# Kernel optimization log

Measured on AMD Instinct MI355X. Metric: run time of the kernel, lower is better.

## Reference

```python
import jax, jax.numpy as jnp
import numpy as np

DEFAULT_MASK_VALUE = -0.7 * float(jnp.finfo(jnp.dtype('float32')).max)

B, T, NQ, NKV, D = 2, 1024, 32, 8, 128


def setup_inputs() -> dict:
    key = jax.random.key(0)
    k1, k2, k3, k4 = jax.random.split(key, 4)
    query = jax.random.normal(k1, (B, T, NQ, D), dtype=jnp.float32)
    kk = jax.random.normal(k2, (B, T, NKV, D), dtype=jnp.float32)
    vv = jax.random.normal(k3, (B, T, NKV, D), dtype=jnp.float32)
    # packed-sequence segment ids, sorted so each segment is contiguous (values 1..3, >0 = active)
    decoder_segment_ids = jnp.sort(jax.random.randint(k4, (B, T), 1, 4), axis=-1).astype(jnp.int32)
    return {"query": query, "key": kk, "value": vv,
            "decoder_segment_ids": decoder_segment_ids}


def _attention(query, key, value, decoder_segment_ids):
    # MaxText AttentionOp.apply_attention_dot (prefill / train mode), GQA layout.
    b, t, n, d = query.shape
    n_kv = key.shape[2]
    g = n // n_kv
    q = query.reshape(b, t, n_kv, g, d)
    # qk product: [b, n_kv, g, t, s]
    logits = jnp.einsum('btkgd,bskd->bkgts', q, key)
    # generate_attention_mask: segment mask AND causal mask
    seg_mask = decoder_segment_ids[:, :, None] == decoder_segment_ids[:, None, :]  # [b,t,s]
    row_ids = jax.lax.broadcasted_iota(jnp.int32, (t, t), 0)
    col_ids = jax.lax.broadcasted_iota(jnp.int32, (t, t), 1)
    causal = col_ids <= row_ids  # [t,s]
    mask = jnp.logical_and(seg_mask, causal[None])  # [b,t,s]
    # apply_mask_to_logits: replace masked entries with DEFAULT_MASK_VALUE (avoids add fusion)
    masked = jnp.where(mask[:, None, None, :, :], logits, DEFAULT_MASK_VALUE)
    probs = jax.nn.softmax(masked, axis=-1)
    out = jnp.einsum('bkgts,bskd->btkgd', probs, value)
    return out.reshape(b, t, n, d)


def reference(query, key, value, decoder_segment_ids):
    return _attention(query, key, value, decoder_segment_ids)
```

## Files before the change

kernel.cpp:

```cpp
#include <hip/hip_runtime.h>

constexpr int B_  = 2;
constexpr int T_  = 1024;
constexpr int NQ  = 32;
constexpr int NKV = 8;
constexpr int D_  = 128;

constexpr int BM = 64;
constexpr int BN = 64;
constexpr int NTILE = T_ / BM;
constexpr float MASK_NEG = -3.0e38f;

typedef _Float16 f16;
typedef __fp16 fp16_2 __attribute__((ext_vector_type(2)));
typedef f16 f16x4 __attribute__((ext_vector_type(4)));
typedef f16 f16x8 __attribute__((ext_vector_type(8)));
typedef float floatx4 __attribute__((ext_vector_type(4)));
typedef unsigned int uintx4 __attribute__((ext_vector_type(4)));

__device__ __align__(16) f16 g_K16 [(size_t)B_ * NKV * T_ * D_];
__device__ __align__(16) f16 g_Vt16[(size_t)B_ * NKV * T_ * D_];

__device__ __forceinline__ void dma16(const f16* g, const f16* l) {
    __builtin_amdgcn_global_load_lds(
        (const __attribute__((address_space(1))) void*)g,
        (__attribute__((address_space(3))) void*)l, 16, 0, 0);
}

__device__ __forceinline__ void swap32(unsigned &a, unsigned &b) {
    unsigned ax = (unsigned)__shfl_xor((int)a, 32);
    unsigned bx = (unsigned)__shfl_xor((int)b, 32);
    const bool hi = (threadIdx.x & 32) != 0;
    unsigned na = hi ? bx : a;
    unsigned nb = hi ? b  : ax;
    a = na; b = nb;
}

__device__ __forceinline__ void swap16(unsigned &a, unsigned &b) {
    unsigned ax = (unsigned)__shfl_xor((int)a, 16);
    unsigned bx = (unsigned)__shfl_xor((int)b, 16);
    const bool odd = (threadIdx.x & 16) != 0;
    unsigned na = odd ? bx : a;
    unsigned nb = odd ? b  : ax;
    a = na; b = nb;
}

__device__ __forceinline__ unsigned pk2(float a, float b) {
    union { fp16_2 h; unsigned u; } c;
    c.h = __builtin_amdgcn_cvt_pkrtz(a, b);
    return c.u;
}

__global__ __launch_bounds__(256)
void prep_kernel(const float* __restrict__ K, const float* __restrict__ V) {
    __shared__ f16 lv[64][136];
    const int sblk = blockIdx.x;
    const int kv   = blockIdx.y;
    const int b    = blockIdx.z;
    const int tid  = threadIdx.x;
    const int s0   = sblk * 64;
    const size_t inbase = ((size_t)b * T_) * NKV * D_ + (size_t)kv * D_;

    f16* kout = g_K16 + ((size_t)(b * NKV + kv) * T_ + s0) * D_;
#pragma unroll
    for (int p = 0; p < 4; ++p) {
        const int u = tid + 256 * p;
        const int s = u >> 4, ch = u & 15;
        const float* src = K + inbase + (size_t)(s0 + s) * NKV * D_ + ch * 8;
        float4 f0 = *(const float4*)src;
        float4 f1 = *(const float4*)(src + 4);
        f16x8 hh;
        hh[0] = (f16)f0.x; hh[1] = (f16)f0.y; hh[2] = (f16)f0.z; hh[3] = (f16)f0.w;
        hh[4] = (f16)f1.x; hh[5] = (f16)f1.y; hh[6] = (f16)f1.z; hh[7] = (f16)f1.w;
        *(f16x8*)(kout + s * D_ + ((ch ^ (s & 7)) * 8)) = hh;
    }
#pragma unroll
    for (int p = 0; p < 8; ++p) {
        const int u = tid + 256 * p;
        const int s = u >> 5, d4 = u & 31;
        float4 f = *(const float4*)(V + inbase + (size_t)(s0 + s) * NKV * D_ + d4 * 4);
        f16x4 hh; hh[0] = (f16)f.x; hh[1] = (f16)f.y; hh[2] = (f16)f.z; hh[3] = (f16)f.w;
        *(f16x4*)&lv[s][d4 * 4] = hh;
    }
    __syncthreads();
    f16* vout = g_Vt16 + (size_t)((b * NKV + kv) * 16 + sblk) * 8192;
#pragma unroll
    for (int p = 0; p < 4; ++p) {
        const int u = tid + 256 * p;
        const int d = u >> 3, cu = u & 7;
        f16x8 hh;
#pragma unroll
        for (int j = 0; j < 8; ++j) hh[j] = lv[cu * 8 + j][d];
        *(f16x8*)(vout + d * 64 + ((cu ^ (d & 7)) * 8)) = hh;
    }
}

#define FA_BODY(RK, RV, WK, WV, blkv)                                          \
    {                                                                          \
        const int s0 = (blkv) * BN;                                            \
        __syncthreads();                                                       \
        if ((blkv) + 1 < nblk) {                                               \
            const f16* kt = kbase + (size_t)((blkv) + 1) * 8192 + glane;       \
            const f16* vt = vbase + (size_t)((blkv) + 1) * 8192 + glane;       \
            _Pragma("unroll")                                                  \
            for (int i = 0; i < 4; ++i) {                                      \
                dma16(kt + i * 512, WK + wbase + i * 512);                     \
                dma16(vt + i * 512, WV + wbase + i * 512);                     \
            }                                                                  \
        }                                                                      \
        floatx4 sc[4];                                                         \
        _Pragma("unroll")                                                      \
        for (int nt = 0; nt < 4; ++nt) {                                       \
            floatx4 acc = floatx4{0.f, 0.f, 0.f, 0.f};                         \
            _Pragma("unroll")                                                  \
            for (int c = 0; c < 4; ++c) {                                      \
                f16x8 kf = *(const f16x8*)(RK + (nt * 16 + ln) * 128 + kpc[c]);\
                acc = __builtin_amdgcn_mfma_f32_16x16x32_f16(kf, qfrag[c], acc, 0, 0, 0); \
            }                                                                  \
            sc[nt] = acc;                                                      \
        }                                                                      \
        _Pragma("unroll")                                                      \
        for (int nt = 0; nt < 4; ++nt) {                                       \
            _Pragma("unroll")                                                  \
            for (int r = 0; r < 4; ++r) {                                      \
                const int s = s0 + nt * 16 + quad * 4 + r;                     \
                const bool ok = (s <= qrow_l) && (s >= fs_l);                  \
                sc[nt][r] = ok ? sc[nt][r] : MASK_NEG;                         \
            }                                                                  \
        }                                                                      \
        float mx = fmaxf(                                                      \
            fmaxf(fmaxf(fmaxf(sc[0][0], sc[0][1]), fmaxf(sc[0][2], sc[0][3])), \
                  fmaxf(fmaxf(sc[1][0], sc[1][1]), fmaxf(sc[1][2], sc[1][3]))),\
            fmaxf(fmaxf(fmaxf(sc[2][0], sc[2][1]), fmaxf(sc[2][2], sc[2][3])), \
                  fmaxf(fmaxf(sc[3][0], sc[3][1]), fmaxf(sc[3][2], sc[3][3]))));\
        mx = fmaxf(mx, __shfl_xor(mx, 16));                                    \
        mx = fmaxf(mx, __shfl_xor(mx, 32));                                    \
        const float mnew = fmaxf(m_i, mx);                                     \
        const float av = __expf(m_i - mnew);                                   \
        m_i = mnew;                                                            \
        _Pragma("unroll")                                                      \
        for (int nt = 0; nt < 4; ++nt) {                                       \
            sc[nt][0] = __expf(sc[nt][0] - mnew);                              \
            sc[nt][1] = __expf(sc[nt][1] - mnew);                              \
            sc[nt][2] = __expf(sc[nt][2] - mnew);                              \
            sc[nt][3] = __expf(sc[nt][3] - mnew);                              \
        }                                                                      \
        const int avi = __float_as_int(av);                                    \
        floatx4 avr;                                                           \
        _Pragma("unroll")                                                      \
        for (int r = 0; r < 4; ++r)                                            \
            avr[r] = __int_as_float(__builtin_amdgcn_ds_bpermute(bpbase + 4 * r, avi)); \
        _Pragma("unroll")                                                      \
        for (int dt = 0; dt < 9; ++dt) o_acc[dt] *= avr;                       \
        unsigned Da[4], Db[4];                                                 \
        _Pragma("unroll")                                                      \
        for (int nt = 0; nt < 4; ++nt) {                                       \
            Da[nt] = pk2(sc[nt][0], sc[nt][1]);                                \
            Db[nt] = pk2(sc[nt][2], sc[nt][3]);                                \
        }                                                                      \
        swap32(Da[0], Da[1]); swap32(Db[0], Db[1]);                            \
        swap16(Da[0], Da[1]); swap16(Db[0], Db[1]);                            \
        swap32(Da[2], Da[3]); swap32(Db[2], Db[3]);                            \
        swap16(Da[2], Da[3]); swap16(Db[2], Db[3]);                            \
        union { uintx4 u; f16x8 h; } c0_, c1_;                                 \
        c0_.u = uintx4{Da[0], Db[0], Da[1], Db[1]};                            \
        c1_.u = uintx4{Da[2], Db[2], Da[3], Db[3]};                            \
        const f16x8 af0 = c0_.h;                                               \
        const f16x8 af1 = c1_.h;                                               \
        _Pragma("unroll")                                                      \
        for (int dt = 0; dt < 8; ++dt) {                                       \
            const f16* vr = RV + (dt * 16 + ln) * 64;                          \
            f16x8 b0 = *(const f16x8*)(vr + pc0);                              \
            f16x8 b1 = *(const f16x8*)(vr + pc1);                              \
            o_acc[dt] = __builtin_amdgcn_mfma_f32_16x16x32_f16(af0, b0, o_acc[dt], 0, 0, 0); \
            o_acc[dt] = __builtin_amdgcn_mfma_f32_16x16x32_f16(af1, b1, o_acc[dt], 0, 0, 0); \
        }                                                                      \
        o_acc[8] = __builtin_amdgcn_mfma_f32_16x16x32_f16(af0, vones, o_acc[8], 0, 0, 0); \
        o_acc[8] = __builtin_amdgcn_mfma_f32_16x16x32_f16(af1, vones, o_acc[8], 0, 0, 0); \
    }

__global__ __launch_bounds__(256, 2)
void fa_kernel(const float* __restrict__ Qg, const int* __restrict__ seg,
               float* __restrict__ Og) {
    __shared__ __align__(16) f16 kb0[64 * 128];
    __shared__ __align__(16) f16 kb1[64 * 128];
    __shared__ __align__(16) f16 vb0[128 * 64];
    __shared__ __align__(16) f16 vb1[128 * 64];
    __shared__ int lds_seg[T_];

    const int pair = blockIdx.x;
    const int h    = blockIdx.y;
    const int b    = blockIdx.z;
    const int kv   = h >> 2;

    const int tid  = threadIdx.x;
    const int wave = tid >> 6;
    const int lane = tid & 63;
    const int quad = lane >> 4;
    const int ln   = lane & 15;
    const int sw   = ln & 7;

    int kpc[4];
#pragma unroll
    for (int c = 0; c < 4; ++c) kpc[c] = ((4 * c + quad) ^ sw) * 8;
    const int pc0 = (quad ^ sw) * 8;
    const int pc1 = ((quad + 4) ^ sw) * 8;
    const int bpbase = quad << 4;

    const int glane = wave * 2048 + lane * 8;
    const int wbase = wave * 2048;

    const f16* kbase = g_K16 + (size_t)(b * NKV + kv) * T_ * D_;
    const f16* vbase = g_Vt16 + (size_t)(b * NKV + kv) * T_ * D_;

    *(int4*)&lds_seg[tid * 4] = *(const int4*)(seg + b * T_ + tid * 4);

    f16x8 vones;
#pragma unroll
    for (int j = 0; j < 8; ++j) vones[j] = (f16)1.0f;

    for (int sub = 0; sub < 2; ++sub) {
        const int tile = sub ? pair : (NTILE - 1 - pair);
        const int t0 = tile * BM;

        const int qrow = t0 + wave * 16 + ln;
        const float* qptr = Qg + (((size_t)b * T_ + qrow) * NQ + h) * D_;
        f16x8 qfrag[4];
#pragma unroll
        for (int c = 0; c < 4; ++c) {
            const float* p = qptr + c * 32 + quad * 8;
            float4 f0 = *(const float4*)(p);
            float4 f1 = *(const float4*)(p + 4);
            f16x8 v;
            v[0] = (f16)f0.x; v[1] = (f16)f0.y; v[2] = (f16)f0.z; v[3] = (f16)f0.w;
            v[4] = (f16)f1.x; v[5] = (f16)f1.y; v[6] = (f16)f1.z; v[7] = (f16)f1.w;
            qfrag[c] = v;
        }

        __syncthreads();

        int trow[4];
#pragma unroll
        for (int r = 0; r < 4; ++r) trow[r] = t0 + wave * 16 + quad * 4 + r;

        const int qrow_l = qrow;
        const int segq_l = lds_seg[qrow_l];
        int lo = 0, hi = qrow_l;
        while (lo < hi) {
            const int mid = (lo + hi) >> 1;
            if (lds_seg[mid] < segq_l) lo = mid + 1; else hi = mid;
        }
        const int fs_l = lo;

        const int seg_lo = lds_seg[t0];
        unsigned long long bal = __ballot(lds_seg[lane * 16 + 15] < seg_lo);
        const int blk_start = __popcll(bal) >> 2;
        const int nblk = tile + 1;

        float  m_i = -1.0e30f;
        floatx4 o_acc[9];
#pragma unroll
        for (int dt = 0; dt < 9; ++dt) o_acc[dt] = floatx4{0.f, 0.f, 0.f, 0.f};

        {
            const f16* kt = kbase + (size_t)blk_start * 8192 + glane;
            const f16* vt = vbase + (size_t)blk_start * 8192 + glane;
#pragma unroll
            for (int i = 0; i < 4; ++i) {
                dma16(kt + i * 512, kb0 + wbase + i * 512);
                dma16(vt + i * 512, vb0 + wbase + i * 512);
            }
        }

        int blk = blk_start;
        while (true) {
            FA_BODY(kb0, vb0, kb1, vb1, blk)
            if (++blk >= nblk) break;
            FA_BODY(kb1, vb1, kb0, vb0, blk)
            if (++blk >= nblk) break;
        }

#pragma unroll
        for (int r = 0; r < 4; ++r) {
            const float inv = 1.0f / o_acc[8][r];
            float* optr = Og + (((size_t)b * T_ + trow[r]) * NQ + h) * D_ + ln;
#pragma unroll
            for (int dt = 0; dt < 8; ++dt)
                optr[dt * 16] = o_acc[dt][r] * inv;
        }
    }
}

extern "C" void kernel_launch(void* const* d_in, const int* in_sizes, int n_in,
                              void* d_out, int out_size, void* d_ws, size_t ws_size,
                              hipStream_t stream) {
    const float* Q   = (const float*)d_in[0];
    const float* K   = (const float*)d_in[1];
    const float* V   = (const float*)d_in[2];
    const int*   seg = (const int*)d_in[3];
    float* out = (float*)d_out;

    dim3 pgrid(NTILE, NKV, B_);
    prep_kernel<<<pgrid, 256, 0, stream>>>(K, V);

    dim3 grid(NTILE / 2, NQ, B_);
    fa_kernel<<<grid, 256, 0, stream>>>(Q, seg, out);
}
```

Measured before the change: 124.6 us.

## Load V directly from global into registers, one tile per block, skip masks/rescales

The attention kernel stops staging V through LDS. Each wave now loads V fragments from global memory into registers and computes PV with transposed 16x16x16 MFMAs, so the score-to-operand lane shuffles and the ones-column row-sum MFMA go away, replaced by an explicit shuffle-reduced l_i. The grid now launches one query tile per block with a rotated tile mapping in place of paired tiles, and occupancy is raised to 4 blocks per SM. The mask is skipped for fully valid blocks, and rescaling is skipped when the running max does not change. The trade-off is higher global/L2 traffic for V and more register pressure in exchange for less LDS use and higher occupancy.

```diff
diff --git a/kernel.cpp b/kernel.cpp
--- a/kernel.cpp
+++ b/kernel.cpp
@@ -16,7 +16,6 @@
 typedef f16 f16x4 __attribute__((ext_vector_type(4)));
 typedef f16 f16x8 __attribute__((ext_vector_type(8)));
 typedef float floatx4 __attribute__((ext_vector_type(4)));
-typedef unsigned int uintx4 __attribute__((ext_vector_type(4)));
 
 __device__ __align__(16) f16 g_K16 [(size_t)B_ * NKV * T_ * D_];
 __device__ __align__(16) f16 g_Vt16[(size_t)B_ * NKV * T_ * D_];
@@ -25,24 +24,6 @@
     __builtin_amdgcn_global_load_lds(
         (const __attribute__((address_space(1))) void*)g,
         (__attribute__((address_space(3))) void*)l, 16, 0, 0);
-}
-
-__device__ __forceinline__ void swap32(unsigned &a, unsigned &b) {
-    unsigned ax = (unsigned)__shfl_xor((int)a, 32);
-    unsigned bx = (unsigned)__shfl_xor((int)b, 32);
-    const bool hi = (threadIdx.x & 32) != 0;
-    unsigned na = hi ? bx : a;
-    unsigned nb = hi ? b  : ax;
-    a = na; b = nb;
-}
-
-__device__ __forceinline__ void swap16(unsigned &a, unsigned &b) {
-    unsigned ax = (unsigned)__shfl_xor((int)a, 16);
-    unsigned bx = (unsigned)__shfl_xor((int)b, 16);
-    const bool odd = (threadIdx.x & 16) != 0;
-    unsigned na = odd ? bx : a;
-    unsigned nb = odd ? b  : ax;
-    a = na; b = nb;
 }
 
 __device__ __forceinline__ unsigned pk2(float a, float b) {
@@ -91,22 +72,28 @@
         f16x8 hh;
 #pragma unroll
         for (int j = 0; j < 8; ++j) hh[j] = lv[cu * 8 + j][d];
-        *(f16x8*)(vout + d * 64 + ((cu ^ (d & 7)) * 8)) = hh;
-    }
-}
-
-#define FA_BODY(RK, RV, WK, WV, blkv)                                          \
+        *(f16x8*)(vout + d * 64 + cu * 8) = hh;
+    }
+}
+
+#define FA_BODY(RK, WK, blkv)                                                  \
     {                                                                          \
         const int s0 = (blkv) * BN;                                            \
         __syncthreads();                                                       \
+                 \
+        const f16* vg = vbase + (size_t)(blkv) * 8192 + vofs;                  \
+        f16x4 vf[8][4];                                                        \
+        _Pragma("unroll")                                                      \
+        for (int dt = 0; dt < 8; ++dt) {                                       \
+            _Pragma("unroll")                                                  \
+            for (int nt = 0; nt < 4; ++nt)                                     \
+                vf[dt][nt] = *(const f16x4*)(vg + dt * 1024 + nt * 16);        \
+        }                                                                      \
         if ((blkv) + 1 < nblk) {                                               \
             const f16* kt = kbase + (size_t)((blkv) + 1) * 8192 + glane;       \
-            const f16* vt = vbase + (size_t)((blkv) + 1) * 8192 + glane;       \
-            _Pragma("unroll")                                                  \
-            for (int i = 0; i < 4; ++i) {                                      \
+            _Pragma("unroll")                                                  \
+            for (int i = 0; i < 4; ++i)                                        \
                 dma16(kt + i * 512, WK + wbase + i * 512);                     \
-                dma16(vt + i * 512, WV + wbase + i * 512);                     \
-            }                                                                  \
         }                                                                      \
         floatx4 sc[4];                                                         \
         _Pragma("unroll")                                                      \
@@ -119,13 +106,17 @@
             }                                                                  \
             sc[nt] = acc;                                                      \
         }                                                                      \
-        _Pragma("unroll")                                                      \
-        for (int nt = 0; nt < 4; ++nt) {                                       \
-            _Pragma("unroll")                                                  \
-            for (int r = 0; r < 4; ++r) {                                      \
-                const int s = s0 + nt * 16 + quad * 4 + r;                     \
-                const bool ok = (s <= qrow_l) && (s >= fs_l);                  \
-                sc[nt][r] = ok ? sc[nt][r] : MASK_NEG;                         \
+        \
+        const bool doMask = !__all((s0 >= fs_l) && (s0 + 63 <= qrow_l));       \
+        if (doMask) {                                                          \
+            _Pragma("unroll")                                                  \
+            for (int nt = 0; nt < 4; ++nt) {                                   \
+                _Pragma("unroll")                                              \
+                for (int r = 0; r < 4; ++r) {                                  \
+                    const int s = s0 + nt * 16 + quad * 4 + r;                 \
+                    const bool ok = (s <= qrow_l) && (s >= fs_l);              \
+                    sc[nt][r] = ok ? sc[nt][r] : MASK_NEG;                     \
+                }                                                              \
             }                                                                  \
         }                                                                      \
         float mx = fmaxf(                                                      \
@@ -136,8 +127,14 @@
         mx = fmaxf(mx, __shfl_xor(mx, 16));                                    \
         mx = fmaxf(mx, __shfl_xor(mx, 32));                                    \
         const float mnew = fmaxf(m_i, mx);                                     \
-        const float av = __expf(m_i - mnew);                                   \
-        m_i = mnew;                                                            \
+                   \
+        if (!__all(mx <= m_i)) {                                               \
+            const float av = __expf(m_i - mnew);                               \
+            m_i = mnew;                                                        \
+            l_i *= av;                                                         \
+            _Pragma("unroll")                                                  \
+            for (int dt = 0; dt < 8; ++dt) o_acc[dt] *= av;                    \
+        }                                                                      \
         _Pragma("unroll")                                                      \
         for (int nt = 0; nt < 4; ++nt) {                                       \
             sc[nt][0] = __expf(sc[nt][0] - mnew);                              \
@@ -145,53 +142,44 @@
             sc[nt][2] = __expf(sc[nt][2] - mnew);                              \
             sc[nt][3] = __expf(sc[nt][3] - mnew);                              \
         }                                                                      \
-        const int avi = __float_as_int(av);                                    \
-        floatx4 avr;                                                           \
-        _Pragma("unroll")                                                      \
-        for (int r = 0; r < 4; ++r)                                            \
-            avr[r] = __int_as_float(__builtin_amdgcn_ds_bpermute(bpbase + 4 * r, avi)); \
-        _Pragma("unroll")                                                      \
-        for (int dt = 0; dt < 9; ++dt) o_acc[dt] *= avr;                       \
-        unsigned Da[4], Db[4];                                                 \
+                                         \
+        floatx4 t01 = sc[0] + sc[1], t23 = sc[2] + sc[3];                      \
+        floatx4 tq  = t01 + t23;                                               \
+        float ts = (tq[0] + tq[1]) + (tq[2] + tq[3]);                          \
+        ts += __shfl_xor(ts, 16);                                              \
+        ts += __shfl_xor(ts, 32);                                              \
+        l_i += ts;                                                             \
+        f16x4 pf[4];                                                           \
         _Pragma("unroll")                                                      \
         for (int nt = 0; nt < 4; ++nt) {                                       \
-            Da[nt] = pk2(sc[nt][0], sc[nt][1]);                                \
-            Db[nt] = pk2(sc[nt][2], sc[nt][3]);                                \
-        }                                                                      \
-        swap32(Da[0], Da[1]); swap32(Db[0], Db[1]);                            \
-        swap16(Da[0], Da[1]); swap16(Db[0], Db[1]);                            \
-        swap32(Da[2], Da[3]); swap32(Db[2], Db[3]);                            \
-        swap16(Da[2], Da[3]); swap16(Db[2], Db[3]);                            \
-        union { uintx4 u; f16x8 h; } c0_, c1_;                                 \
-        c0_.u = uintx4{Da[0], Db[0], Da[1], Db[1]};                            \
-        c1_.u = uintx4{Da[2], Db[2], Da[3], Db[3]};                            \
-        const f16x8 af0 = c0_.h;                                               \
-        const f16x8 af1 = c1_.h;                                               \
+            union { unsigned u[2]; f16x4 h; } pu;                              \
+            pu.u[0] = pk2(sc[nt][0], sc[nt][1]);                               \
+            pu.u[1] = pk2(sc[nt][2], sc[nt][3]);                               \
+            pf[nt] = pu.h;                                                     \
+        }                                                                      \
+        __builtin_amdgcn_s_setprio(1);                                         \
         _Pragma("unroll")                                                      \
         for (int dt = 0; dt < 8; ++dt) {                                       \
-            const f16* vr = RV + (dt * 16 + ln) * 64;                          \
-            f16x8 b0 = *(const f16x8*)(vr + pc0);                              \
-            f16x8 b1 = *(const f16x8*)(vr + pc1);                              \
-            o_acc[dt] = __builtin_amdgcn_mfma_f32_16x16x32_f16(af0, b0, o_acc[dt], 0, 0, 0); \
-            o_acc[dt] = __builtin_amdgcn_mfma_f32_16x16x32_f16(af1, b1, o_acc[dt], 0, 0, 0); \
-        }                                                                      \
-        o_acc[8] = __builtin_amdgcn_mfma_f32_16x16x32_f16(af0, vones, o_acc[8], 0, 0, 0); \
-        o_acc[8] = __builtin_amdgcn_mfma_f32_16x16x32_f16(af1, vones, o_acc[8], 0, 0, 0); \
-    }
-
-__global__ __launch_bounds__(256, 2)
+            _Pragma("unroll")                                                  \
+            for (int nt = 0; nt < 4; ++nt)                                     \
+                o_acc[dt] = __builtin_amdgcn_mfma_f32_16x16x16f16(vf[dt][nt], pf[nt], o_acc[dt], 0, 0, 0); \
+        }                                                                      \
+        __builtin_amdgcn_s_setprio(0);                                         \
+    }
+
+__global__ __launch_bounds__(256, 4)
 void fa_kernel(const float* __restrict__ Qg, const int* __restrict__ seg,
                float* __restrict__ Og) {
     __shared__ __align__(16) f16 kb0[64 * 128];
     __shared__ __align__(16) f16 kb1[64 * 128];
-    __shared__ __align__(16) f16 vb0[128 * 64];
-    __shared__ __align__(16) f16 vb1[128 * 64];
     __shared__ int lds_seg[T_];
 
-    const int pair = blockIdx.x;
-    const int h    = blockIdx.y;
-    const int b    = blockIdx.z;
-    const int kv   = h >> 2;
+    const int x = blockIdx.x, y = blockIdx.y, b = blockIdx.z;
+    int u = (x + (y & 15)) & 15;
+    if (b) u = (u + 8) & 15;
+    const int tile = (y & 16) ? (15 - u) : u;
+    const int h  = y;
+    const int kv = h >> 2;
 
     const int tid  = threadIdx.x;
     const int wave = tid >> 6;
@@ -203,9 +191,7 @@
     int kpc[4];
 #pragma unroll
     for (int c = 0; c < 4; ++c) kpc[c] = ((4 * c + quad) ^ sw) * 8;
-    const int pc0 = (quad ^ sw) * 8;
-    const int pc1 = ((quad + 4) ^ sw) * 8;
-    const int bpbase = quad << 4;
+    const int vofs = ln * 64 + quad * 4;
 
     const int glane = wave * 2048 + lane * 8;
     const int wbase = wave * 2048;
@@ -215,78 +201,66 @@
 
     *(int4*)&lds_seg[tid * 4] = *(const int4*)(seg + b * T_ + tid * 4);
 
-    f16x8 vones;
-#pragma unroll
-    for (int j = 0; j < 8; ++j) vones[j] = (f16)1.0f;
-
-    for (int sub = 0; sub < 2; ++sub) {
-        const int tile = sub ? pair : (NTILE - 1 - pair);
-        const int t0 = tile * BM;
-
-        const int qrow = t0 + wave * 16 + ln;
-        const float* qptr = Qg + (((size_t)b * T_ + qrow) * NQ + h) * D_;
-        f16x8 qfrag[4];
-#pragma unroll
-        for (int c = 0; c < 4; ++c) {
-            const float* p = qptr + c * 32 + quad * 8;
-            float4 f0 = *(const float4*)(p);
-            float4 f1 = *(const float4*)(p + 4);
-            f16x8 v;
-            v[0] = (f16)f0.x; v[1] = (f16)f0.y; v[2] = (f16)f0.z; v[3] = (f16)f0.w;
-            v[4] = (f16)f1.x; v[5] = (f16)f1.y; v[6] = (f16)f1.z; v[7] = (f16)f1.w;
-            qfrag[c] = v;
-        }
-
-        __syncthreads();
-
-        int trow[4];
-#pragma unroll
-        for (int r = 0; r < 4; ++r) trow[r] = t0 + wave * 16 + quad * 4 + r;
-
-        const int qrow_l = qrow;
-        const int segq_l = lds_seg[qrow_l];
-        int lo = 0, hi = qrow_l;
-        while (lo < hi) {
-            const int mid = (lo + hi) >> 1;
-            if (lds_seg[mid] < segq_l) lo = mid + 1; else hi = mid;
-        }
-        const int fs_l = lo;
-
-        const int seg_lo = lds_seg[t0];
-        unsigned long long bal = __ballot(lds_seg[lane * 16 + 15] < seg_lo);
-        const int blk_start = __popcll(bal) >> 2;
-        const int nblk = tile + 1;
-
-        float  m_i = -1.0e30f;
-        floatx4 o_acc[9];
-#pragma unroll
-        for (int dt = 0; dt < 9; ++dt) o_acc[dt] = floatx4{0.f, 0.f, 0.f, 0.f};
-
-        {
-            const f16* kt = kbase + (size_t)blk_start * 8192 + glane;
-            const f16* vt = vbase + (size_t)blk_start * 8192 + glane;
-#pragma unroll
-            for (int i = 0; i < 4; ++i) {
-                dma16(kt + i * 512, kb0 + wbase + i * 512);
-                dma16(vt + i * 512, vb0 + wbase + i * 512);
-            }
-        }
-
-        int blk = blk_start;
-        while (true) {
-            FA_BODY(kb0, vb0, kb1, vb1, blk)
-            if (++blk >= nblk) break;
-            FA_BODY(kb1, vb1, kb0, vb0, blk)
-            if (++blk >= nblk) break;
-        }
-
-#pragma unroll
-        for (int r = 0; r < 4; ++r) {
-            const float inv = 1.0f / o_acc[8][r];
-            float* optr = Og + (((size_t)b * T_ + trow[r]) * NQ + h) * D_ + ln;
-#pragma unroll
-            for (int dt = 0; dt < 8; ++dt)
-                optr[dt * 16] = o_acc[dt][r] * inv;
+    const int t0 = tile * BM;
+
+    const int qrow_l = t0 + wave * 16 + ln;
+    const float* qptr = Qg + (((size_t)b * T_ + qrow_l) * NQ + h) * D_;
+    f16x8 qfrag[4];
+#pragma unroll
+    for (int c = 0; c < 4; ++c) {
+        const float* p = qptr + c * 32 + quad * 8;
+        float4 f0 = *(const float4*)(p);
+        float4 f1 = *(const float4*)(p + 4);
+        f16x8 v;
+        v[0] = (f16)f0.x; v[1] = (f16)f0.y; v[2] = (f16)f0.z; v[3] = (f16)f0.w;
+        v[4] = (f16)f1.x; v[5] = (f16)f1.y; v[6] = (f16)f1.z; v[7] = (f16)f1.w;
+        qfrag[c] = v;
+    }
+
+    __syncthreads();
+
+    const int segq = lds_seg[qrow_l];
+    int lo = 0, hi = qrow_l;
+    while (lo < hi) {
+        const int mid = (lo + hi) >> 1;
+        if (lds_seg[mid] < segq) lo = mid + 1; else hi = mid;
+    }
+    const int fs_l = lo;
+
+    const int seg_lo = lds_seg[t0];
+    unsigned long long bal = __ballot(lds_seg[lane * 16 + 15] < seg_lo);
+    const int blk_start = __popcll(bal) >> 2;
+    const int nblk = tile + 1;
+
+    float  m_i = -1.0e30f;
+    float  l_i = 0.f;
+    floatx4 o_acc[8];
+#pragma unroll
+    for (int dt = 0; dt < 8; ++dt) o_acc[dt] = floatx4{0.f, 0.f, 0.f, 0.f};
+
+    {
+        const f16* kt = kbase + (size_t)blk_start * 8192 + glane;
+#pragma unroll
+        for (int i = 0; i < 4; ++i)
+            dma16(kt + i * 512, kb0 + wbase + i * 512);
+    }
+
+    int blk = blk_start;
+    while (true) {
+        FA_BODY(kb0, kb1, blk)
+        if (++blk >= nblk) break;
+        FA_BODY(kb1, kb0, blk)
+        if (++blk >= nblk) break;
+    }
+
+    {
+        const float inv = 1.0f / l_i;
+        float* optr = Og + (((size_t)b * T_ + qrow_l) * NQ + h) * D_;
+#pragma unroll
+        for (int dt = 0; dt < 8; ++dt) {
+            floatx4 o = o_acc[dt];
+            o[0] *= inv; o[1] *= inv; o[2] *= inv; o[3] *= inv;
+            *(floatx4*)(optr + dt * 16 + quad * 4) = o;
         }
     }
 }
@@ -300,9 +274,9 @@
     const int*   seg = (const int*)d_in[3];
     float* out = (float*)d_out;
 
-    dim3 pgrid(NTILE, NKV, B_);
+    dim3 pgrid(16, NKV, B_);
     prep_kernel<<<pgrid, 256, 0, stream>>>(K, V);
 
-    dim3 grid(NTILE / 2, NQ, B_);
+    dim3 grid(NTILE, NQ, B_);
     fa_kernel<<<grid, 256, 0, stream>>>(Q, seg, out);
 }
```

Measured after the change: 193.2 us. +55.0%, slower.
